# Kernel optimization log

Measured on AMD Instinct MI355X. Metric: run time of the kernel, lower is better.

The kernel has to match this reference:

```python
import jax, jax.numpy as jnp
import numpy as np

N = 50000   # num nodes
E = 800000  # num edges (avg degree 16)
D = 128     # in = hidden = out channels


def setup_inputs() -> dict:
    key = jax.random.key(0)
    k0, k1, k2, k3, k4, k5 = jax.random.split(key, 6)
    x = jax.random.normal(k0, (N, D), dtype=jnp.float32)
    edge_index = jax.random.randint(k1, (2, E), 0, N, dtype=jnp.int32)
    scale = 1.0 / np.sqrt(D)
    W1 = jax.random.normal(k2, (D, D), dtype=jnp.float32) * scale
    b1 = jax.random.normal(k3, (D,), dtype=jnp.float32) * 0.01
    W2 = jax.random.normal(k4, (D, D), dtype=jnp.float32) * scale
    b2 = jax.random.normal(k5, (D,), dtype=jnp.float32) * 0.01
    return {"x": x, "edge_index": edge_index, "W1": W1, "b1": b1, "W2": W2, "b2": b2}


def reference(x, edge_index, W1, b1, W2, b2):
    n = x.shape[0]
    src, dst = edge_index[0], edge_index[1]
    # GCN adds self-loops before normalization
    loops = jnp.arange(n, dtype=src.dtype)
    s = jnp.concatenate([src, loops])
    d = jnp.concatenate([dst, loops])
    # symmetric normalization: deg^{-1/2}[s] * deg^{-1/2}[d]
    deg = jax.ops.segment_sum(jnp.ones_like(d, dtype=x.dtype), d, num_segments=n)
    dinv = jnp.where(deg > 0, jax.lax.rsqrt(deg), 0.0)
    ew = dinv[s] * dinv[d]  # [E+N]

    def gcn_conv(h, W, b):
        h = h @ W                                   # [N, D] dense transform first
        msg = ew[:, None] * h[s]                     # gather over edges [E+N, D]
        agg = jax.ops.segment_sum(msg, d, num_segments=n)  # scatter-add [N, D]
        return agg + b

    # layer 1: conv -> Identity BN -> ELU (dropout=0.0 -> no-op)
    h = jax.nn.elu(gcn_conv(x, W1, b1))
    # layer 2 (last): conv -> Identity BN -> ELU
    out = jax.nn.elu(gcn_conv(h, W2, b2))
    return out
```

## Files before the change

### kernel.cpp

```cpp
#include <hip/hip_runtime.h>
#include <math.h>

#define D 128
#define BCAP 8192
#define SLICE 64
#define PB 256

typedef __attribute__((ext_vector_type(8))) short bf16x8;
typedef __attribute__((ext_vector_type(4))) float f32x4;
typedef __attribute__((ext_vector_type(4))) unsigned int u32x4;


__device__ inline float2 bf2f2(unsigned int u) {
    union { unsigned int i; float f; } a, b;
    a.i = u << 16;
    b.i = u & 0xffff0000u;
    return make_float2(a.f, b.f);
}

__device__ inline unsigned short f2bf(float f) {
    union { float f; unsigned int i; } u;
    u.f = f;
    unsigned int r = u.i + 0x7fffu + ((u.i >> 16) & 1u);
    return (unsigned short)(r >> 16);
}

__device__ __forceinline__ float elu_fast(float r) {
    return r > 0.f ? r : __expf(r) - 1.f;
}


__device__ __forceinline__ void gemm_core(unsigned short (*Ws)[136], int gbid,
                                          const void* __restrict__ Ain, int a_fp32,
                                          unsigned int* __restrict__ Cb, int N) {
    const int tid = threadIdx.x;
    const int wid = tid >> 6;
    const int lane = tid & 63;
    const int quad = lane >> 4;
    const int ln = lane & 15;
    const int m = gbid * 64 + wid * 16 + ln;
    const bool valid = (m < N);

    f32x4 acc[8];
#pragma unroll
    for (int c = 0; c < 8; ++c) acc[c] = (f32x4){0.f, 0.f, 0.f, 0.f};

    __syncthreads();

#pragma unroll
    for (int ks = 0; ks < 4; ++ks) {
        const int k0 = ks * 32;
        bf16x8 af;
        if (a_fp32) {
            const float* A = (const float*)Ain;
            float4 lo = make_float4(0.f, 0.f, 0.f, 0.f), hi = lo;
            if (valid) {
                lo = *(const float4*)&A[(size_t)m * 128 + k0 + quad * 8];
                hi = *(const float4*)&A[(size_t)m * 128 + k0 + quad * 8 + 4];
            }
            af[0] = (short)f2bf(lo.x); af[1] = (short)f2bf(lo.y);
            af[2] = (short)f2bf(lo.z); af[3] = (short)f2bf(lo.w);
            af[4] = (short)f2bf(hi.x); af[5] = (short)f2bf(hi.y);
            af[6] = (short)f2bf(hi.z); af[7] = (short)f2bf(hi.w);
        } else {
            const uint4* A4 = (const uint4*)Ain;
            uint4 v = valid ? A4[(size_t)m * 16 + ks * 4 + quad]
                            : make_uint4(0u, 0u, 0u, 0u);
            union { uint4 u; bf16x8 h; } cv;
            cv.u = v;
            af = cv.h;
        }
#pragma unroll
        for (int c = 0; c < 8; ++c) {
            bf16x8 bf = *(const bf16x8*)&Ws[c * 16 + ln][k0 + quad * 8];
            acc[c] = __builtin_amdgcn_mfma_f32_16x16x32_bf16(af, bf, acc[c], 0, 0, 0);
        }
    }

    const int rowbase = gbid * 64 + wid * 16 + quad * 4;
#pragma unroll
    for (int c = 0; c < 8; ++c) {
#pragma unroll
        for (int r = 0; r < 4; ++r) {
            float v = acc[c][r];
            float vn = __shfl_xor(v, 1);
            int grow = rowbase + r;
            if (!(ln & 1) && grow < N) {
                unsigned int u = (unsigned int)f2bf(v) | ((unsigned int)f2bf(vn) << 16);
                Cb[(size_t)grow * 64 + c * 8 + (ln >> 1)] = u;
            }
        }
    }
}


__global__ __launch_bounds__(256) void k1_part(
        const int* __restrict__ src, const int* __restrict__ dst,
        unsigned int* __restrict__ pairs, unsigned char* __restrict__ cellCnt,
        int e, int chunk) {
    __shared__ int cur[256];
    const int tid = threadIdx.x;
    const int bid = blockIdx.x;
    cur[tid] = 0;
    __syncthreads();
    const int e0 = bid * chunk;
    const int e1 = min(e0 + chunk, e);
    for (int i = e0 + tid; i < e1; i += 256) {
        int d = dst[i], s = src[i];
        int b = d >> 8;
        int off = atomicAdd(&cur[b], 1);
        if (off < SLICE)
            pairs[((size_t)(b * 256 + bid)) * SLICE + off] =
                (unsigned int)s | ((unsigned int)(d & 255) << 16);
    }
    __syncthreads();
    cellCnt[(size_t)tid * 256 + bid] = (unsigned char)min(cur[tid], SLICE);
}


__global__ __launch_bounds__(256) void k1_gemm(
        const float* __restrict__ x, const float* __restrict__ W1,
        const float* __restrict__ W2, unsigned short* __restrict__ Wt2,
        unsigned int* __restrict__ hb1, int N, int gemmBlocks) {
    __shared__ __align__(16) unsigned short Ws[128][136];
    const int tid = threadIdx.x;
    const int bid = blockIdx.x;

    if (bid < gemmBlocks) {
#pragma unroll
        for (int j = 0; j < 16; ++j) {
            const int q = tid + j * 256;
            const float4 w = ((const float4*)W1)[q];
            const int k = q >> 5;
            const int n0 = (q & 31) * 4;
            Ws[n0 + 0][k] = f2bf(w.x);
            Ws[n0 + 1][k] = f2bf(w.y);
            Ws[n0 + 2][k] = f2bf(w.z);
            Ws[n0 + 3][k] = f2bf(w.w);
        }
        gemm_core(Ws, bid, x, 1, hb1, N);
    } else {
        int i = (bid - gemmBlocks) * 256 + tid;
        int k = i >> 7, n = i & 127;
        Wt2[n * 128 + k] = f2bf(W2[i]);
    }
}


__global__ __launch_bounds__(1024) void partB(const unsigned int* __restrict__ pairs,
                                              const unsigned char* __restrict__ cellCnt,
                                              unsigned short* __restrict__ col,
                                              unsigned int* __restrict__ meta,
                                              float* __restrict__ dinv, int n) {
    __shared__ unsigned int cellS[256 * SLICE];
    __shared__ int cnt[256];
    __shared__ int deg[256];
    __shared__ int sc[256];
    __shared__ int cur[256];
    const int b = blockIdx.x;
    const int tid = threadIdx.x;
    const int ch = tid >> 2;
    const int sub = tid & 3;

    {
        const uint4* gp = (const uint4*)(pairs + (size_t)b * (256 * SLICE));
        uint4* sp = (uint4*)cellS;
#pragma unroll
        for (int r = 0; r < 4; ++r) sp[tid + r * 1024] = gp[tid + r * 1024];
    }
    if (tid < 256) {
        cnt[tid] = min((int)cellCnt[(size_t)b * 256 + tid], SLICE);
        deg[tid] = 0;
    }
    __syncthreads();

    const int c = cnt[ch];
    for (int q = sub; q < c; q += 4) atomicAdd(&deg[cellS[ch * SLICE + q] >> 16], 1);
    __syncthreads();

    if (tid < 256) sc[tid] = deg[tid];
    __syncthreads();
    for (int o = 1; o < 256; o <<= 1) {
        int t = 0;
        if (tid < 256 && tid >= o) t = sc[tid - o];
        __syncthreads();
        if (tid < 256) sc[tid] += t;
        __syncthreads();
    }
    if (tid < 256) {
        int v = deg[tid];
        int startw = sc[tid] - v;
        cur[tid] = startw;
        int node = b * 256 + tid;
        if (node < n) {
            meta[node] = ((unsigned int)(b * BCAP + startw) << 10) | (unsigned int)v;
            dinv[node] = rsqrtf((float)(v + 1));
        }
    }
    __syncthreads();

    for (int q = sub; q < c; q += 4) {
        unsigned int p = cellS[ch * SLICE + q];
        int dl = p >> 16;
        int off = atomicAdd(&cur[dl], 1);
        col[(size_t)b * BCAP + off] = (unsigned short)(p & 0xffffu);
    }
}


__device__ __forceinline__ void fma8(float w, u32x4 u, f32x4& a, f32x4& b) {
    float2 v0 = bf2f2(u.x), v1 = bf2f2(u.y), v2 = bf2f2(u.z), v3 = bf2f2(u.w);
    a[0] = fmaf(w, v0.x, a[0]); a[1] = fmaf(w, v0.y, a[1]);
    a[2] = fmaf(w, v1.x, a[2]); a[3] = fmaf(w, v1.y, a[3]);
    b[0] = fmaf(w, v2.x, b[0]); b[1] = fmaf(w, v2.y, b[1]);
    b[2] = fmaf(w, v3.x, b[2]); b[3] = fmaf(w, v3.y, b[3]);
}

__device__ __forceinline__ void add8(u32x4 u, f32x4& a, f32x4& b) {
    float2 v0 = bf2f2(u.x), v1 = bf2f2(u.y), v2 = bf2f2(u.z), v3 = bf2f2(u.w);
    a[0] += v0.x; a[1] += v0.y; a[2] += v1.x; a[3] += v1.y;
    b[0] += v2.x; b[1] += v2.y; b[2] += v3.x; b[3] += v3.y;
}

template <bool PRE>
__device__ __forceinline__ float2 agg_wave_rs(const unsigned int* __restrict__ hb,
                                              const unsigned short* __restrict__ col,
                                              const float* __restrict__ dinv,
                                              int node, int g, int ln,
                                              unsigned int m, float di) {
    const u32x4* hb4 = (const u32x4*)hb;
    const int s0 = (int)(m >> 10);
    const int s1 = s0 + (int)(m & 1023u);

    f32x4 sA = (f32x4){0.f, 0.f, 0.f, 0.f};
    f32x4 sB = (f32x4){0.f, 0.f, 0.f, 0.f};
    {
        u32x4 su = hb4[((unsigned)node << 4) + ln];
        float ws = (g == 0) ? (PRE ? 1.f : di) : 0.f;
        fma8(ws, su, sA, sB);
    }

    int i = s0;
    for (; i + 16 <= s1; i += 16) {
        const int c0 = col[i + g];
        const int c1 = col[i + 4 + g];
        const int c2 = col[i + 8 + g];
        const int c3 = col[i + 12 + g];
        float w0 = 0.f, w1 = 0.f, w2 = 0.f, w3 = 0.f;
        if (!PRE) { w0 = dinv[c0]; w1 = dinv[c1]; w2 = dinv[c2]; w3 = dinv[c3]; }
        u32x4 u0 = hb4[((unsigned)c0 << 4) + ln];
        u32x4 u1 = hb4[((unsigned)c1 << 4) + ln];
        u32x4 u2 = hb4[((unsigned)c2 << 4) + ln];
        u32x4 u3 = hb4[((unsigned)c3 << 4) + ln];
        asm volatile("" :: "v"(u0), "v"(u1), "v"(u2), "v"(u3));
        if (PRE) {
            add8(u0, sA, sB); add8(u1, sA, sB);
            add8(u2, sA, sB); add8(u3, sA, sB);
        } else {
            fma8(w0, u0, sA, sB); fma8(w1, u1, sA, sB);
            fma8(w2, u2, sA, sB); fma8(w3, u3, sA, sB);
        }
    }
    while (i < s1) {
        const int t = i + g;
        const bool ok = (t < s1);
        const int cc = ok ? (int)col[t] : node;
        u32x4 u = hb4[((unsigned)cc << 4) + ln];
        if (PRE) {
            if (ok) add8(u, sA, sB);
        } else {
            const float w = ok ? dinv[cc] : 0.f;
            fma8(w, u, sA, sB);
        }
        i += 4;
    }

    f32x4 t;
#pragma unroll
    for (int k = 0; k < 4; ++k) {
        float pa = __shfl_xor(sA[k], 16);
        float pb = __shfl_xor(sB[k], 16);
        t[k] = (g & 1) ? (sB[k] + pb) : (sA[k] + pa);
    }
    float p0 = __shfl_xor(t[0], 32);
    float p1 = __shfl_xor(t[1], 32);
    float p2 = __shfl_xor(t[2], 32);
    float p3 = __shfl_xor(t[3], 32);
    float e0 = (g & 2) ? (t[2] + p2) : (t[0] + p0);
    float e1 = (g & 2) ? (t[3] + p3) : (t[1] + p1);
    return make_float2(e0, e1);
}


__global__ __launch_bounds__(1024, 4) void k3_agg_gemm(
        const unsigned int* __restrict__ hb1, const unsigned int* __restrict__ meta,
        const unsigned short* __restrict__ col, const float* __restrict__ dinv,
        const float* __restrict__ b1, const unsigned short* __restrict__ Wt2,
        unsigned int* __restrict__ hb2, int n) {
    __shared__ unsigned int g1s[16 * 68];
    __shared__ __align__(16) unsigned short Ws[128][136];

    const int tid = threadIdx.x;
    const int wid = tid >> 6;
    const int lane = tid & 63;
    const int g = lane >> 4;
    const int ln = lane & 15;
    const int nodeBase = blockIdx.x * 16;
    const int node = nodeBase + wid;

    {
        const int nloc = tid >> 3;
        const int kb = (tid & 7) * 16;
        const uint4* gp = (const uint4*)(Wt2 + (size_t)nloc * 128 + kb);
        uint4* sp = (uint4*)&Ws[nloc][kb];
        sp[0] = gp[0];
        sp[1] = gp[1];
    }

    const int cp = 4 * ln + 2 * (g & 1) + (g >> 1);
    if (node < n) {
        const unsigned int m = meta[node];
        const float di = dinv[node];
        float2 e = agg_wave_rs<false>(hb1, col, dinv, node, g, ln, m, di);
        const float2 bv = ((const float2*)b1)[cp];
        float r0 = elu_fast(fmaf(di, e.x, bv.x));
        float r1 = elu_fast(fmaf(di, e.y, bv.y));
        g1s[wid * 68 + cp] = (unsigned int)f2bf(r0) | ((unsigned int)f2bf(r1) << 16);
    } else {
        g1s[wid * 68 + cp] = 0u;
    }
    __syncthreads();

    if (wid < 8) {
        const int quad = lane >> 4;
        f32x4 acc = (f32x4){0.f, 0.f, 0.f, 0.f};
#pragma unroll
        for (int ks = 0; ks < 4; ++ks) {
            bf16x8 af = *(const bf16x8*)&g1s[ln * 68 + ks * 16 + quad * 4];
            bf16x8 bf = *(const bf16x8*)&Ws[wid * 16 + ln][ks * 32 + quad * 8];
            acc = __builtin_amdgcn_mfma_f32_16x16x32_bf16(af, bf, acc, 0, 0, 0);
        }
#pragma unroll
        for (int r = 0; r < 4; ++r) {
            int grow = nodeBase + quad * 4 + r;
            float dsc = (grow < n) ? dinv[grow] : 0.f;
            float v = acc[r] * dsc;
            float vn = __shfl_xor(v, 1);
            if (!(ln & 1) && grow < n) {
                hb2[(size_t)grow * 64 + wid * 8 + (ln >> 1)] =
                    (unsigned int)f2bf(v) | ((unsigned int)f2bf(vn) << 16);
            }
        }
    }
}


__global__ __launch_bounds__(256, 4) void agg_elu(const unsigned int* __restrict__ hb,
                                                  const unsigned int* __restrict__ meta,
                                                  const unsigned short* __restrict__ col,
                                                  const float* __restrict__ dinv,
                                                  const float* __restrict__ bias,
                                                  float* __restrict__ outf, int n) {
    const int wid = threadIdx.x >> 6;
    const int lane = threadIdx.x & 63;
    const int g = lane >> 4;
    const int ln = lane & 15;
    const int node = blockIdx.x * 4 + wid;
    if (node >= n) return;

    const unsigned int m = meta[node];
    const float di = dinv[node];
    float2 e = agg_wave_rs<true>(hb, col, dinv, node, g, ln, m, di);

    const int cp = 4 * ln + 2 * (g & 1) + (g >> 1);
    const float2 bv = ((const float2*)bias)[cp];
    float2 r;
    r.x = elu_fast(fmaf(di, e.x, bv.x));
    r.y = elu_fast(fmaf(di, e.y, bv.y));
    ((float2*)outf)[(size_t)node * 64 + cp] = r;
}


extern "C" void kernel_launch(void* const* d_in, const int* in_sizes, int n_in,
                              void* d_out, int out_size, void* d_ws, size_t ws_size,
                              hipStream_t stream) {
    const float* x  = (const float*)d_in[0];
    const int*   ei = (const int*)d_in[1];
    const float* W1 = (const float*)d_in[2];
    const float* b1 = (const float*)d_in[3];
    const float* W2 = (const float*)d_in[4];
    const float* b2 = (const float*)d_in[5];
    float* out = (float*)d_out;

    const int N = in_sizes[0] / D;
    const int E = in_sizes[1] / 2;
    const int* src = ei;
    const int* dst = ei + E;
    const int NB = (N + 255) / 256;

    char* ws = (char*)d_ws;
    size_t off = 0;
    auto alloc = [&](size_t bytes) -> void* {
        void* p = ws + off;
        off = (off + bytes + 255) & ~(size_t)255;
        return p;
    };
    unsigned int*   pairs   = (unsigned int*)alloc((size_t)256 * PB * SLICE * 4);
    unsigned char*  cellCnt = (unsigned char*)alloc((size_t)256 * PB);
    unsigned short* col     = (unsigned short*)alloc((size_t)NB * BCAP * 2);
    unsigned int*   meta    = (unsigned int*)alloc((size_t)N * 4);
    float*          dinv    = (float*)alloc((size_t)N * 4);
    unsigned short* Wt2     = (unsigned short*)alloc(128 * 128 * 2);
    unsigned int*   hb1     = (unsigned int*)alloc((size_t)N * 64 * 4);
    unsigned int*   hb2     = (unsigned int*)alloc((size_t)N * 64 * 4);
    (void)ws_size; (void)n_in; (void)out_size;

    const int chunk = (E + PB - 1) / PB;
    const int gemmBlocks = (N + 63) / 64;

    k1_part<<<PB, 256, 0, stream>>>(src, dst, pairs, cellCnt, E, chunk);
    k1_gemm<<<gemmBlocks + 64, 256, 0, stream>>>(x, W1, W2, Wt2, hb1, N, gemmBlocks);
    partB<<<NB, 1024, 0, stream>>>(pairs, cellCnt, col, meta, dinv, N);
    k3_agg_gemm<<<(N + 15) / 16, 1024, 0, stream>>>(hb1, meta, col, dinv, b1, Wt2, hb2, N);
    agg_elu<<<(N + 3) / 4, 256, 0, stream>>>(hb2, meta, col, dinv, b2, out, N);
}
```

Measured before the change: 198.1 us.

## Merge partition and GEMM launches; batch aggregation tail into one predicated pass

The edge partition kernel and the first-layer GEMM/W2-transpose kernel are merged into a single launch, with blocks dispatched by index and sharing one LDS buffer. This removes a launch and lets the two independent phases run concurrently. The aggregation loop now stops the unrolled main body earlier and handles the remaining up to 31 neighbours plus the self-loop in one fully predicated batch of 8 gathers, replacing the serial 4-at-a-time tail. That raises memory-level parallelism for low-degree nodes, at the cost of more registers and extra masked loads.

```diff
diff --git a/kernel.cpp b/kernel.cpp
--- a/kernel.cpp
+++ b/kernel.cpp
@@ -94,39 +94,34 @@
 }
 
 
-__global__ __launch_bounds__(256) void k1_part(
+__global__ __launch_bounds__(256) void k1_all(
         const int* __restrict__ src, const int* __restrict__ dst,
+        const float* __restrict__ x, const float* __restrict__ W1,
+        const float* __restrict__ W2, unsigned short* __restrict__ Wt2,
         unsigned int* __restrict__ pairs, unsigned char* __restrict__ cellCnt,
-        int e, int chunk) {
-    __shared__ int cur[256];
+        unsigned int* __restrict__ hb1, int e, int chunk, int N, int gemmBlocks) {
+    __shared__ __align__(16) unsigned char smem[128 * 136 * 2];
     const int tid = threadIdx.x;
     const int bid = blockIdx.x;
-    cur[tid] = 0;
-    __syncthreads();
-    const int e0 = bid * chunk;
-    const int e1 = min(e0 + chunk, e);
-    for (int i = e0 + tid; i < e1; i += 256) {
-        int d = dst[i], s = src[i];
-        int b = d >> 8;
-        int off = atomicAdd(&cur[b], 1);
-        if (off < SLICE)
-            pairs[((size_t)(b * 256 + bid)) * SLICE + off] =
-                (unsigned int)s | ((unsigned int)(d & 255) << 16);
-    }
-    __syncthreads();
-    cellCnt[(size_t)tid * 256 + bid] = (unsigned char)min(cur[tid], SLICE);
-}
-
-
-__global__ __launch_bounds__(256) void k1_gemm(
-        const float* __restrict__ x, const float* __restrict__ W1,
-        const float* __restrict__ W2, unsigned short* __restrict__ Wt2,
-        unsigned int* __restrict__ hb1, int N, int gemmBlocks) {
-    __shared__ __align__(16) unsigned short Ws[128][136];
-    const int tid = threadIdx.x;
-    const int bid = blockIdx.x;
-
-    if (bid < gemmBlocks) {
+
+    if (bid < PB) {
+        int* cur = (int*)smem;
+        cur[tid] = 0;
+        __syncthreads();
+        const int e0 = bid * chunk;
+        const int e1 = min(e0 + chunk, e);
+        for (int i = e0 + tid; i < e1; i += 256) {
+            int d = dst[i], s = src[i];
+            int b = d >> 8;
+            int off = atomicAdd(&cur[b], 1);
+            if (off < SLICE)
+                pairs[((size_t)(b * 256 + bid)) * SLICE + off] =
+                    (unsigned int)s | ((unsigned int)(d & 255) << 16);
+        }
+        __syncthreads();
+        cellCnt[(size_t)tid * 256 + bid] = (unsigned char)min(cur[tid], SLICE);
+    } else if (bid < PB + gemmBlocks) {
+        unsigned short (*Ws)[136] = (unsigned short(*)[136])smem;
 #pragma unroll
         for (int j = 0; j < 16; ++j) {
             const int q = tid + j * 256;
@@ -138,9 +133,9 @@
             Ws[n0 + 2][k] = f2bf(w.z);
             Ws[n0 + 3][k] = f2bf(w.w);
         }
-        gemm_core(Ws, bid, x, 1, hb1, N);
+        gemm_core(Ws, bid - PB, x, 1, hb1, N);
     } else {
-        int i = (bid - gemmBlocks) * 256 + tid;
+        int i = (bid - PB - gemmBlocks) * 256 + tid;
         int k = i >> 7, n = i & 127;
         Wt2[n * 128 + k] = f2bf(W2[i]);
     }
@@ -216,12 +211,6 @@
     b[2] = fmaf(w, v3.x, b[2]); b[3] = fmaf(w, v3.y, b[3]);
 }
 
-__device__ __forceinline__ void add8(u32x4 u, f32x4& a, f32x4& b) {
-    float2 v0 = bf2f2(u.x), v1 = bf2f2(u.y), v2 = bf2f2(u.z), v3 = bf2f2(u.w);
-    a[0] += v0.x; a[1] += v0.y; a[2] += v1.x; a[3] += v1.y;
-    b[0] += v2.x; b[1] += v2.y; b[2] += v3.x; b[3] += v3.y;
-}
-
 template <bool PRE>
 __device__ __forceinline__ float2 agg_wave_rs(const unsigned int* __restrict__ hb,
                                               const unsigned short* __restrict__ col,
@@ -234,45 +223,64 @@
 
     f32x4 sA = (f32x4){0.f, 0.f, 0.f, 0.f};
     f32x4 sB = (f32x4){0.f, 0.f, 0.f, 0.f};
-    {
-        u32x4 su = hb4[((unsigned)node << 4) + ln];
-        float ws = (g == 0) ? (PRE ? 1.f : di) : 0.f;
-        fma8(ws, su, sA, sB);
-    }
+
+    u32x4 su = hb4[((unsigned)node << 4) + ln];
 
     int i = s0;
-    for (; i + 16 <= s1; i += 16) {
+    while (i + 32 <= s1) {
         const int c0 = col[i + g];
         const int c1 = col[i + 4 + g];
         const int c2 = col[i + 8 + g];
         const int c3 = col[i + 12 + g];
-        float w0 = 0.f, w1 = 0.f, w2 = 0.f, w3 = 0.f;
+        float w0 = 1.f, w1 = 1.f, w2 = 1.f, w3 = 1.f;
         if (!PRE) { w0 = dinv[c0]; w1 = dinv[c1]; w2 = dinv[c2]; w3 = dinv[c3]; }
         u32x4 u0 = hb4[((unsigned)c0 << 4) + ln];
         u32x4 u1 = hb4[((unsigned)c1 << 4) + ln];
         u32x4 u2 = hb4[((unsigned)c2 << 4) + ln];
         u32x4 u3 = hb4[((unsigned)c3 << 4) + ln];
         asm volatile("" :: "v"(u0), "v"(u1), "v"(u2), "v"(u3));
-        if (PRE) {
-            add8(u0, sA, sB); add8(u1, sA, sB);
-            add8(u2, sA, sB); add8(u3, sA, sB);
-        } else {
-            fma8(w0, u0, sA, sB); fma8(w1, u1, sA, sB);
-            fma8(w2, u2, sA, sB); fma8(w3, u3, sA, sB);
-        }
-    }
-    while (i < s1) {
-        const int t = i + g;
-        const bool ok = (t < s1);
-        const int cc = ok ? (int)col[t] : node;
-        u32x4 u = hb4[((unsigned)cc << 4) + ln];
-        if (PRE) {
-            if (ok) add8(u, sA, sB);
-        } else {
-            const float w = ok ? dinv[cc] : 0.f;
-            fma8(w, u, sA, sB);
-        }
-        i += 4;
+        fma8(w0, u0, sA, sB); fma8(w1, u1, sA, sB);
+        fma8(w2, u2, sA, sB); fma8(w3, u3, sA, sB);
+        i += 16;
+    }
+
+    {
+        const int t0 = i + g,       t1 = i + 4 + g;
+        const int t2 = i + 8 + g,   t3 = i + 12 + g;
+        const int t4 = i + 16 + g,  t5 = i + 20 + g;
+        const int t6 = i + 24 + g,  t7 = i + 28 + g;
+        const int c0 = (t0 < s1) ? (int)col[t0] : node;
+        const int c1 = (t1 < s1) ? (int)col[t1] : node;
+        const int c2 = (t2 < s1) ? (int)col[t2] : node;
+        const int c3 = (t3 < s1) ? (int)col[t3] : node;
+        const int c4 = (t4 < s1) ? (int)col[t4] : node;
+        const int c5 = (t5 < s1) ? (int)col[t5] : node;
+        const int c6 = (t6 < s1) ? (int)col[t6] : node;
+        const int c7 = (t7 < s1) ? (int)col[t7] : node;
+        const float w0 = (t0 < s1) ? (PRE ? 1.f : dinv[c0]) : 0.f;
+        const float w1 = (t1 < s1) ? (PRE ? 1.f : dinv[c1]) : 0.f;
+        const float w2 = (t2 < s1) ? (PRE ? 1.f : dinv[c2]) : 0.f;
+        const float w3 = (t3 < s1) ? (PRE ? 1.f : dinv[c3]) : 0.f;
+        const float w4 = (t4 < s1) ? (PRE ? 1.f : dinv[c4]) : 0.f;
+        const float w5 = (t5 < s1) ? (PRE ? 1.f : dinv[c5]) : 0.f;
+        const float w6 = (t6 < s1) ? (PRE ? 1.f : dinv[c6]) : 0.f;
+        const float w7 = (t7 < s1) ? (PRE ? 1.f : dinv[c7]) : 0.f;
+        u32x4 u0 = hb4[((unsigned)c0 << 4) + ln];
+        u32x4 u1 = hb4[((unsigned)c1 << 4) + ln];
+        u32x4 u2 = hb4[((unsigned)c2 << 4) + ln];
+        u32x4 u3 = hb4[((unsigned)c3 << 4) + ln];
+        u32x4 u4 = hb4[((unsigned)c4 << 4) + ln];
+        u32x4 u5 = hb4[((unsigned)c5 << 4) + ln];
+        u32x4 u6 = hb4[((unsigned)c6 << 4) + ln];
+        u32x4 u7 = hb4[((unsigned)c7 << 4) + ln];
+        asm volatile("" :: "v"(u0), "v"(u1), "v"(u2), "v"(u3),
+                          "v"(u4), "v"(u5), "v"(u6), "v"(u7), "v"(su));
+        const float ws = (g == 0) ? (PRE ? 1.f : di) : 0.f;
+        fma8(ws, su, sA, sB);
+        fma8(w0, u0, sA, sB); fma8(w1, u1, sA, sB);
+        fma8(w2, u2, sA, sB); fma8(w3, u3, sA, sB);
+        fma8(w4, u4, sA, sB); fma8(w5, u5, sA, sB);
+        fma8(w6, u6, sA, sB); fma8(w7, u7, sA, sB);
     }
 
     f32x4 t;
@@ -418,8 +426,9 @@
     const int chunk = (E + PB - 1) / PB;
     const int gemmBlocks = (N + 63) / 64;
 
-    k1_part<<<PB, 256, 0, stream>>>(src, dst, pairs, cellCnt, E, chunk);
-    k1_gemm<<<gemmBlocks + 64, 256, 0, stream>>>(x, W1, W2, Wt2, hb1, N, gemmBlocks);
+    k1_all<<<PB + gemmBlocks + 64, 256, 0, stream>>>(src, dst, x, W1, W2, Wt2,
+                                                     pairs, cellCnt, hb1, E, chunk,
+                                                     N, gemmBlocks);
     partB<<<NB, 1024, 0, stream>>>(pairs, cellCnt, col, meta, dinv, N);
     k3_agg_gemm<<<(N + 15) / 16, 1024, 0, stream>>>(hb1, meta, col, dinv, b1, Wt2, hb2, N);
     agg_elu<<<(N + 3) / 4, 256, 0, stream>>>(hb2, meta, col, dinv, b2, out, N);
```

New measurement: 192.5 us. 2.9% less time.

## Merge partition and GEMM kernels; process two nodes per wave in final aggregation

Applied to the files above, without the earlier changes.

Fuses the edge-partition kernel and the first GEMM/W2-transpose kernel into one launch, with the block index selecting the role and shared memory reused between roles. This removes a launch boundary and lets the two independent phases overlap. The final aggregation kernel is rewritten so each wave handles two nodes, with half-waves assigned per node and 8 edges per iteration. Stores become float4 and the cross-lane reduction is shorter. The template specialization is removed. The risk is imbalance when the two paired nodes have different degrees, since the loop runs to the larger of the two.

```diff
diff --git a/kernel.cpp b/kernel.cpp
--- a/kernel.cpp
+++ b/kernel.cpp
@@ -94,39 +94,34 @@
 }
 
 
-__global__ __launch_bounds__(256) void k1_part(
+__global__ __launch_bounds__(256) void k1_all(
         const int* __restrict__ src, const int* __restrict__ dst,
+        const float* __restrict__ x, const float* __restrict__ W1,
+        const float* __restrict__ W2, unsigned short* __restrict__ Wt2,
         unsigned int* __restrict__ pairs, unsigned char* __restrict__ cellCnt,
-        int e, int chunk) {
-    __shared__ int cur[256];
+        unsigned int* __restrict__ hb1, int e, int chunk, int N, int gemmBlocks) {
+    __shared__ __align__(16) unsigned char smem[128 * 136 * 2];
     const int tid = threadIdx.x;
     const int bid = blockIdx.x;
-    cur[tid] = 0;
-    __syncthreads();
-    const int e0 = bid * chunk;
-    const int e1 = min(e0 + chunk, e);
-    for (int i = e0 + tid; i < e1; i += 256) {
-        int d = dst[i], s = src[i];
-        int b = d >> 8;
-        int off = atomicAdd(&cur[b], 1);
-        if (off < SLICE)
-            pairs[((size_t)(b * 256 + bid)) * SLICE + off] =
-                (unsigned int)s | ((unsigned int)(d & 255) << 16);
-    }
-    __syncthreads();
-    cellCnt[(size_t)tid * 256 + bid] = (unsigned char)min(cur[tid], SLICE);
-}
-
-
-__global__ __launch_bounds__(256) void k1_gemm(
-        const float* __restrict__ x, const float* __restrict__ W1,
-        const float* __restrict__ W2, unsigned short* __restrict__ Wt2,
-        unsigned int* __restrict__ hb1, int N, int gemmBlocks) {
-    __shared__ __align__(16) unsigned short Ws[128][136];
-    const int tid = threadIdx.x;
-    const int bid = blockIdx.x;
-
-    if (bid < gemmBlocks) {
+
+    if (bid < PB) {
+        int* cur = (int*)smem;
+        cur[tid] = 0;
+        __syncthreads();
+        const int e0 = bid * chunk;
+        const int e1 = min(e0 + chunk, e);
+        for (int i = e0 + tid; i < e1; i += 256) {
+            int d = dst[i], s = src[i];
+            int b = d >> 8;
+            int off = atomicAdd(&cur[b], 1);
+            if (off < SLICE)
+                pairs[((size_t)(b * 256 + bid)) * SLICE + off] =
+                    (unsigned int)s | ((unsigned int)(d & 255) << 16);
+        }
+        __syncthreads();
+        cellCnt[(size_t)tid * 256 + bid] = (unsigned char)min(cur[tid], SLICE);
+    } else if (bid < PB + gemmBlocks) {
+        unsigned short (*Ws)[136] = (unsigned short(*)[136])smem;
 #pragma unroll
         for (int j = 0; j < 16; ++j) {
             const int q = tid + j * 256;
@@ -138,9 +133,9 @@
             Ws[n0 + 2][k] = f2bf(w.z);
             Ws[n0 + 3][k] = f2bf(w.w);
         }
-        gemm_core(Ws, bid, x, 1, hb1, N);
+        gemm_core(Ws, bid - PB, x, 1, hb1, N);
     } else {
-        int i = (bid - gemmBlocks) * 256 + tid;
+        int i = (bid - PB - gemmBlocks) * 256 + tid;
         int k = i >> 7, n = i & 127;
         Wt2[n * 128 + k] = f2bf(W2[i]);
     }
@@ -222,7 +217,6 @@
     b[0] += v2.x; b[1] += v2.y; b[2] += v3.x; b[3] += v3.y;
 }
 
-template <bool PRE>
 __device__ __forceinline__ float2 agg_wave_rs(const unsigned int* __restrict__ hb,
                                               const unsigned short* __restrict__ col,
                                               const float* __restrict__ dinv,
@@ -236,7 +230,7 @@
     f32x4 sB = (f32x4){0.f, 0.f, 0.f, 0.f};
     {
         u32x4 su = hb4[((unsigned)node << 4) + ln];
-        float ws = (g == 0) ? (PRE ? 1.f : di) : 0.f;
+        float ws = (g == 0) ? di : 0.f;
         fma8(ws, su, sA, sB);
     }
 
@@ -246,32 +240,22 @@
         const int c1 = col[i + 4 + g];
         const int c2 = col[i + 8 + g];
         const int c3 = col[i + 12 + g];
-        float w0 = 0.f, w1 = 0.f, w2 = 0.f, w3 = 0.f;
-        if (!PRE) { w0 = dinv[c0]; w1 = dinv[c1]; w2 = dinv[c2]; w3 = dinv[c3]; }
+        const float w0 = dinv[c0], w1 = dinv[c1], w2 = dinv[c2], w3 = dinv[c3];
         u32x4 u0 = hb4[((unsigned)c0 << 4) + ln];
         u32x4 u1 = hb4[((unsigned)c1 << 4) + ln];
         u32x4 u2 = hb4[((unsigned)c2 << 4) + ln];
         u32x4 u3 = hb4[((unsigned)c3 << 4) + ln];
         asm volatile("" :: "v"(u0), "v"(u1), "v"(u2), "v"(u3));
-        if (PRE) {
-            add8(u0, sA, sB); add8(u1, sA, sB);
-            add8(u2, sA, sB); add8(u3, sA, sB);
-        } else {
-            fma8(w0, u0, sA, sB); fma8(w1, u1, sA, sB);
-            fma8(w2, u2, sA, sB); fma8(w3, u3, sA, sB);
-        }
+        fma8(w0, u0, sA, sB); fma8(w1, u1, sA, sB);
+        fma8(w2, u2, sA, sB); fma8(w3, u3, sA, sB);
     }
     while (i < s1) {
         const int t = i + g;
         const bool ok = (t < s1);
         const int cc = ok ? (int)col[t] : node;
+        const float w = ok ? dinv[cc] : 0.f;
         u32x4 u = hb4[((unsigned)cc << 4) + ln];
-        if (PRE) {
-            if (ok) add8(u, sA, sB);
-        } else {
-            const float w = ok ? dinv[cc] : 0.f;
-            fma8(w, u, sA, sB);
-        }
+        fma8(w, u, sA, sB);
         i += 4;
     }
 
@@ -321,7 +305,7 @@
     if (node < n) {
         const unsigned int m = meta[node];
         const float di = dinv[node];
-        float2 e = agg_wave_rs<false>(hb1, col, dinv, node, g, ln, m, di);
+        float2 e = agg_wave_rs(hb1, col, dinv, node, g, ln, m, di);
         const float2 bv = ((const float2*)b1)[cp];
         float r0 = elu_fast(fmaf(di, e.x, bv.x));
         float r1 = elu_fast(fmaf(di, e.y, bv.y));
@@ -355,29 +339,81 @@
 }
 
 
-__global__ __launch_bounds__(256, 4) void agg_elu(const unsigned int* __restrict__ hb,
-                                                  const unsigned int* __restrict__ meta,
-                                                  const unsigned short* __restrict__ col,
-                                                  const float* __restrict__ dinv,
-                                                  const float* __restrict__ bias,
-                                                  float* __restrict__ outf, int n) {
+__global__ __launch_bounds__(256, 4) void agg_elu2(
+        const unsigned int* __restrict__ hb, const unsigned int* __restrict__ meta,
+        const unsigned short* __restrict__ col, const float* __restrict__ dinv,
+        const float* __restrict__ bias, float* __restrict__ outf, int n) {
     const int wid = threadIdx.x >> 6;
     const int lane = threadIdx.x & 63;
-    const int g = lane >> 4;
+    const int h = lane >> 5;
+    const int q = (lane >> 4) & 1;
     const int ln = lane & 15;
-    const int node = blockIdx.x * 4 + wid;
-    if (node >= n) return;
-
-    const unsigned int m = meta[node];
-    const float di = dinv[node];
-    float2 e = agg_wave_rs<true>(hb, col, dinv, node, g, ln, m, di);
-
-    const int cp = 4 * ln + 2 * (g & 1) + (g >> 1);
-    const float2 bv = ((const float2*)bias)[cp];
-    float2 r;
-    r.x = elu_fast(fmaf(di, e.x, bv.x));
-    r.y = elu_fast(fmaf(di, e.y, bv.y));
-    ((float2*)outf)[(size_t)node * 64 + cp] = r;
+    const int nb = (blockIdx.x * 4 + wid) * 2;
+    if (nb >= n) return;
+    const int node = nb + h;
+    const bool valid = (node < n);
+    const int selfrow = valid ? node : nb;
+
+    const unsigned int m0 = meta[nb];
+    const unsigned int m1 = (nb + 1 < n) ? meta[nb + 1] : 0u;
+    const unsigned int mh = h ? m1 : m0;
+    const int s0 = (int)(mh >> 10);
+    const int s1 = s0 + (int)(mh & 1023u);
+    const int dmax = max((int)(m0 & 1023u), (int)(m1 & 1023u));
+    const int R = (dmax + 7) >> 3;
+
+    const u32x4* hb4 = (const u32x4*)hb;
+    const float dih = dinv[selfrow];
+
+    f32x4 sA = (f32x4){0.f, 0.f, 0.f, 0.f};
+    f32x4 sB = (f32x4){0.f, 0.f, 0.f, 0.f};
+    {
+        u32x4 su = hb4[((unsigned)selfrow << 4) + ln];
+        if (q == 0 && valid) add8(su, sA, sB);
+    }
+
+    for (int r = 0; r < R; ++r) {
+        const int base = s0 + r * 8;
+        const int t0 = base + 0 + q;
+        const int t1 = base + 2 + q;
+        const int t2 = base + 4 + q;
+        const int t3 = base + 6 + q;
+        const int c0 = (t0 < s1) ? (int)col[t0] : selfrow;
+        const int c1 = (t1 < s1) ? (int)col[t1] : selfrow;
+        const int c2 = (t2 < s1) ? (int)col[t2] : selfrow;
+        const int c3 = (t3 < s1) ? (int)col[t3] : selfrow;
+        u32x4 u0 = hb4[((unsigned)c0 << 4) + ln];
+        u32x4 u1 = hb4[((unsigned)c1 << 4) + ln];
+        u32x4 u2 = hb4[((unsigned)c2 << 4) + ln];
+        u32x4 u3 = hb4[((unsigned)c3 << 4) + ln];
+        asm volatile("" :: "v"(u0), "v"(u1), "v"(u2), "v"(u3));
+        if (t0 < s1) add8(u0, sA, sB);
+        if (t1 < s1) add8(u1, sA, sB);
+        if (t2 < s1) add8(u2, sA, sB);
+        if (t3 < s1) add8(u3, sA, sB);
+    }
+
+#pragma unroll
+    for (int k = 0; k < 4; ++k) {
+        sA[k] += __shfl_xor(sA[k], 16);
+        sB[k] += __shfl_xor(sB[k], 16);
+    }
+
+    if (q == 0 && valid) {
+        const float4 bA = ((const float4*)bias)[2 * ln];
+        const float4 bB = ((const float4*)bias)[2 * ln + 1];
+        float4 rA, rB;
+        rA.x = elu_fast(fmaf(dih, sA[0], bA.x));
+        rA.y = elu_fast(fmaf(dih, sA[1], bA.y));
+        rA.z = elu_fast(fmaf(dih, sA[2], bA.z));
+        rA.w = elu_fast(fmaf(dih, sA[3], bA.w));
+        rB.x = elu_fast(fmaf(dih, sB[0], bB.x));
+        rB.y = elu_fast(fmaf(dih, sB[1], bB.y));
+        rB.z = elu_fast(fmaf(dih, sB[2], bB.z));
+        rB.w = elu_fast(fmaf(dih, sB[3], bB.w));
+        ((float4*)outf)[(size_t)node * 32 + 2 * ln] = rA;
+        ((float4*)outf)[(size_t)node * 32 + 2 * ln + 1] = rB;
+    }
 }
 
 
@@ -418,9 +454,10 @@
     const int chunk = (E + PB - 1) / PB;
     const int gemmBlocks = (N + 63) / 64;
 
-    k1_part<<<PB, 256, 0, stream>>>(src, dst, pairs, cellCnt, E, chunk);
-    k1_gemm<<<gemmBlocks + 64, 256, 0, stream>>>(x, W1, W2, Wt2, hb1, N, gemmBlocks);
+    k1_all<<<PB + gemmBlocks + 64, 256, 0, stream>>>(src, dst, x, W1, W2, Wt2,
+                                                     pairs, cellCnt, hb1, E, chunk,
+                                                     N, gemmBlocks);
     partB<<<NB, 1024, 0, stream>>>(pairs, cellCnt, col, meta, dinv, N);
     k3_agg_gemm<<<(N + 15) / 16, 1024, 0, stream>>>(hb1, meta, col, dinv, b1, Wt2, hb2, N);
-    agg_elu<<<(N + 3) / 4, 256, 0, stream>>>(hb2, meta, col, dinv, b2, out, N);
-}
+    agg_elu2<<<(N + 7) / 8, 256, 0, stream>>>(hb2, meta, col, dinv, b2, out, N);
+}
```

After: 192.5 us. 1.03x faster.
